# Kernel optimization log

Hardware: AMD Instinct MI355X
Metric: run time of the kernel (lower is better)

The kernel has to match this reference:

```python
import jax, jax.numpy as jnp
import numpy as np

NUM_HEADS = 16
H_SELF = 10  # hardcoded h in forward: first 10 heads self-attend, rest cross-attend
DIM = 1024
HEAD_DIM = DIM // NUM_HEADS
SCALE = HEAD_DIM ** -0.5


def _qkv(x, Wqkv):
    # x: [B, N, C] -> q, k, v each [B, H, N, hd]
    B, N, C = x.shape
    qkv = (x @ Wqkv).reshape(B, N, 3, NUM_HEADS, C // NUM_HEADS).transpose(2, 0, 3, 1, 4)
    return qkv[0], qkv[1], qkv[2]


def _attn(q, k, v):
    # q,k,v: [B, h, N, d]
    scores = jnp.einsum('bhqd,bhkd->bhqk', q, k) * SCALE
    probs = jax.nn.softmax(scores, axis=-1)  # attn_drop_ratio = 0.0
    return jnp.einsum('bhqk,bhkd->bhqd', probs, v)


def _proj(xa, xb, Wproj, bproj):
    # xa: [B, 10, N, d], xb: [B, 6, N, d] -> [B, N, C]
    B = xa.shape[0]
    N = xa.shape[2]
    x = jnp.concatenate([xa, xb], axis=1).transpose(0, 2, 1, 3).reshape(B, N, DIM)
    return x @ Wproj + bproj  # proj_drop_ratio = 0.0


def setup_inputs() -> dict:
    key = jax.random.key(0)
    k0, k1, k2, k3 = jax.random.split(key, 4)
    B, N, C = 16, 577, DIM
    x1 = jax.random.normal(k0, (B, N, C), dtype=jnp.float32)
    x2 = jax.random.normal(k1, (B, N, C), dtype=jnp.float32)
    # nn.Linear(dim, dim*3, bias=False): store as [C, 3C] so y = x @ W
    Wqkv = jax.random.normal(k2, (C, 3 * C), dtype=jnp.float32) * 0.02
    # nn.Linear(dim, dim) has bias by default
    Wproj = jax.random.normal(k3, (C, C), dtype=jnp.float32) * 0.02
    bproj = jnp.zeros((C,), dtype=jnp.float32)
    return {"x1": x1, "x2": x2, "Wqkv": Wqkv, "Wproj": Wproj, "bproj": bproj}


def reference(x1, x2, Wqkv, Wproj, bproj):
    q1, k1, v1 = _qkv(x1, Wqkv)
    q2, k2, v2 = _qkv(x2, Wqkv)
    h = H_SELF
    x11 = _attn(q1[:, :h], k1[:, :h], v1[:, :h])  # self-attn branch of x1
    x12 = _attn(q1[:, h:], k2[:, h:], v2[:, h:])  # cross: q from x1, kv from x2
    x22 = _attn(q2[:, :h], k2[:, :h], v2[:, :h])  # self-attn branch of x2
    x21 = _attn(q2[:, h:], k1[:, h:], v1[:, h:])  # cross: q from x2, kv from x1
    out1 = _proj(x11, x12, Wproj, bproj)
    out2 = _proj(x22, x21, Wproj, bproj)
    return (out1, out2)
```

## Files before the change

kernel.cpp:

```cpp
#include <hip/hip_runtime.h>
#include <hip/hip_bf16.h>
#include <stdint.h>
#include <math.h>

typedef __attribute__((ext_vector_type(8))) short bf16x8;
typedef __attribute__((ext_vector_type(4))) float f32x4;
typedef __attribute__((ext_vector_type(8))) unsigned short ushort8;
typedef __attribute__((ext_vector_type(4))) unsigned int uint4v;
typedef __attribute__((ext_vector_type(2))) unsigned int uint2v;

#define NTOK   9232
#define MROWS  18464
#define MPAD   18560
#define NPADV  640
#define QSCALE 0.18033688011112042f

__device__ __forceinline__ uint16_t f2b(float f) {
  uint32_t u = __builtin_bit_cast(uint32_t, f);
  u += 0x7fffu + ((u >> 16) & 1u);
  return (uint16_t)(u >> 16);
}

__device__ __forceinline__ uint32_t packbf(float lo, float hi) {
  return (uint32_t)f2b(lo) | ((uint32_t)f2b(hi) << 16);
}

__device__ __forceinline__ f32x4 mfma16(bf16x8 a, bf16x8 b, f32x4 c) {
  return __builtin_amdgcn_mfma_f32_16x16x32_bf16(a, b, c, 0, 0, 0);
}

__device__ __forceinline__ void gl_lds16(const void* g, void* l) {
  __builtin_amdgcn_global_load_lds(
      (const __attribute__((address_space(1))) uint32_t*)g,
      (__attribute__((address_space(3))) uint32_t*)l, 16, 0, 0);
}

__global__ void convert_x_kernel(const float* __restrict__ x1,
                                 const float* __restrict__ x2,
                                 uint16_t* __restrict__ Xb) {
  const size_t stride = (size_t)gridDim.x * blockDim.x;
  const size_t total8 = (size_t)MPAD * 1024 / 8;
  for (size_t i = (size_t)blockIdx.x * blockDim.x + threadIdx.x; i < total8; i += stride) {
    const size_t e = i * 8;
    const size_t row = e >> 10;
    ushort8 ov;
    if (row < (size_t)MROWS) {
      const float* src = (row < (size_t)NTOK) ? (x1 + e) : (x2 + (e - (size_t)NTOK * 1024));
      float4 a = *(const float4*)(src);
      float4 b = *(const float4*)(src + 4);
      ov[0] = f2b(a.x); ov[1] = f2b(a.y); ov[2] = f2b(a.z); ov[3] = f2b(a.w);
      ov[4] = f2b(b.x); ov[5] = f2b(b.y); ov[6] = f2b(b.z); ov[7] = f2b(b.w);
    } else {
      ov = (ushort8)0;
    }
    *(ushort8*)(Xb + e) = ov;
  }
}

__global__ void transw_kernel(const float* __restrict__ in, uint16_t* __restrict__ out,
                              int R, int Cc) {
  __shared__ float t[32][33];
  const int r0 = blockIdx.x * 32, c0 = blockIdx.y * 32;
  const int tr = threadIdx.x >> 5, tc = threadIdx.x & 31;
#pragma unroll
  for (int i = 0; i < 4; ++i)
    t[tr + i * 8][tc] = in[(size_t)(r0 + tr + i * 8) * Cc + c0 + tc];
  __syncthreads();
#pragma unroll
  for (int i = 0; i < 4; ++i) {
    const int orow = c0 + tr + i * 8;
    out[(size_t)orow * R + r0 + tc] = f2b(t[tc][tr + i * 8]);
  }
}

__global__ __launch_bounds__(256) void gemm_qkv_kernel(
    const uint16_t* __restrict__ A, const uint16_t* __restrict__ Bt,
    uint16_t* __restrict__ Qb, uint16_t* __restrict__ Kb, uint16_t* __restrict__ Vtb) {
  __shared__ uint16_t As[128 * 32];
  __shared__ uint16_t Bs[128 * 32];
  const int tid = threadIdx.x;
  const int w = tid >> 6, l = tid & 63;
  const int c = l & 15, g = l >> 4;
  const int wgid = blockIdx.x;
  const int work = (wgid & 7) * 435 + (wgid >> 3);
  int bm, bn;
  {
    const int stripe = work / 144;
    if (stripe >= 24) { bm = 144; bn = work - 24 * 144; }
    else {
      const int r2 = work % 144;
      const int st8 = r2 / 48, r3 = r2 % 48;
      bm = stripe * 6 + r3 % 6;
      bn = st8 * 8 + r3 / 6;
    }
  }
  const int wm = w >> 1, wn = w & 1;
  f32x4 acc[4][4] = {};

  const int srow = w * 32 + (l >> 2);
  const int scolB = (l & 3) * 16;
  const char* aG = (const char*)(A + (size_t)bm * 128 * 1024);
  const char* bG = (const char*)(Bt + (size_t)bn * 128 * 1024);
  char* aL0 = (char*)As + srow * 64 + scolB;
  char* aL1 = (char*)As + (srow + 16) * 64 + scolB;
  char* bL0 = (char*)Bs + srow * 64 + scolB;
  char* bL1 = (char*)Bs + (srow + 16) * 64 + scolB;
  const char* aG0 = aG + (size_t)srow * 2048 + scolB;
  const char* aG1 = aG + (size_t)(srow + 16) * 2048 + scolB;
  const char* bG0 = bG + (size_t)srow * 2048 + scolB;
  const char* bG1 = bG + (size_t)(srow + 16) * 2048 + scolB;

  for (int ks = 0; ks < 1024; ks += 32) {
    gl_lds16(aG0 + ks * 2, aL0);
    gl_lds16(aG1 + ks * 2, aL1);
    gl_lds16(bG0 + ks * 2, bL0);
    gl_lds16(bG1 + ks * 2, bL1);
    __syncthreads();
    bf16x8 af[4], bfv[4];
#pragma unroll
    for (int mi = 0; mi < 4; ++mi)
      af[mi] = *(const bf16x8*)((const char*)As + (wm * 64 + mi * 16 + c) * 64 + g * 16);
#pragma unroll
    for (int ni = 0; ni < 4; ++ni)
      bfv[ni] = *(const bf16x8*)((const char*)Bs + (wn * 64 + ni * 16 + c) * 64 + g * 16);
#pragma unroll
    for (int mi = 0; mi < 4; ++mi)
#pragma unroll
      for (int ni = 0; ni < 4; ++ni)
        acc[mi][ni] = mfma16(af[mi], bfv[ni], acc[mi][ni]);
    __syncthreads();
  }

  const int sArea = bn >> 3;
#pragma unroll
  for (int mi = 0; mi < 4; ++mi) {
#pragma unroll
    for (int r = 0; r < 4; ++r) {
      const int R = bm * 128 + wm * 64 + mi * 16 + g * 4 + r;
      if (R >= MROWS) continue;
      const int src = (R >= NTOK) ? 1 : 0;
      const int rr = R - src * NTOK;
      const int bb = rr / 577;
      const int nn = rr - bb * 577;
#pragma unroll
      for (int ni = 0; ni < 4; ++ni) {
        const int C = bn * 128 + wn * 64 + ni * 16 + c;
        const int c10 = C & 1023;
        const int hh = c10 >> 6, dd = c10 & 63;
        const size_t bh = ((size_t)src * 16 + bb) * 16 + hh;
        const float v = acc[mi][ni][r];
        if (sArea == 0)
          Qb[(bh * 577 + nn) * 64 + dd] = f2b(v * QSCALE);
        else if (sArea == 1)
          Kb[(bh * 577 + nn) * 64 + dd] = f2b(v);
        else
          Vtb[(bh * 64 + dd) * NPADV + nn] = f2b(v);
      }
    }
  }
}

#define KVB 64
#define ATT_NT 10
__global__ __launch_bounds__(256, 2) void attn_kernel(
    const uint16_t* __restrict__ Qb, const uint16_t* __restrict__ Kb,
    const uint16_t* __restrict__ Vtb, uint16_t* __restrict__ O) {
  __shared__ __align__(128) char smem[65536];
  const int tid = threadIdx.x;
  const int w = tid >> 6, l = tid & 63;
  const int c = l & 15, g = l >> 4;
  const int bid = blockIdx.x;
  const int qc = bid % 3;
  const int p = bid / 3;
  const int h = p & 15, b = (p >> 4) & 15, o = p >> 8;
  const int kvsrc = (h < 10) ? o : (1 - o);
  const uint16_t* qp = Qb + (((size_t)o * 16 + b) * 16 + h) * 577 * 64;
  const uint16_t* kp = Kb + (((size_t)kvsrc * 16 + b) * 16 + h) * 577 * 64;
  const uint16_t* vp = Vtb + (((size_t)kvsrc * 16 + b) * 16 + h) * 64 * NPADV;

  const int qbase = qc * 256 + w * 64;
  const bool active = (qbase <= 576);

  const int sub = l >> 3;
  const int colEl = (((l & 7) ^ sub) << 3);
  char* KsA = smem;
  char* VsA = smem + 16384;
  char* Pb  = smem + 32768 + w * 8192;
  const int rs = (c & 7) << 4;

  bf16x8 Qf[4][2];
  if (active) {
#pragma unroll
    for (int qt = 0; qt < 4; ++qt) {
      const int qrow = min(qbase + qt * 16 + c, 576);
      const uint16_t* qr = qp + (size_t)qrow * 64 + g * 8;
      Qf[qt][0] = *(const bf16x8*)(qr);
      Qf[qt][1] = *(const bf16x8*)(qr + 32);
    }
  }

  f32x4 acc[4][4] = {};
  float m_run[4] = {-3.0e38f, -3.0e38f, -3.0e38f, -3.0e38f};
  float l_run[4] = {0.f, 0.f, 0.f, 0.f};

  auto STAGE = [&](int buf, int kv0) {
#pragma unroll
    for (int i = 0; i < 2; ++i) {
      const int j = w * 2 + i;
      const int row = j * 8 + sub;
      const int gk = min(kv0 + row, 576);
      gl_lds16(kp + (size_t)gk * 64 + colEl, KsA + buf * 8192 + j * 1024 + l * 16);
      gl_lds16(vp + (size_t)row * NPADV + kv0 + colEl, VsA + buf * 8192 + j * 1024 + l * 16);
    }
  };

  STAGE(0, 0);
  __syncthreads();

  for (int t = 0; t < ATT_NT; ++t) {
    if (t < ATT_NT - 1) STAGE((t + 1) & 1, (t + 1) * KVB);
    if (active) {
      const char* Kt = KsA + (t & 1) * 8192;
      const char* Vt = VsA + (t & 1) * 8192;
      bf16x8 Kf[4][2];
#pragma unroll
      for (int kt = 0; kt < 4; ++kt) {
        const char* kr = Kt + (kt * 16 + c) * 128;
        Kf[kt][0] = *(const bf16x8*)(kr + ((g * 16) ^ rs));
        Kf[kt][1] = *(const bf16x8*)(kr + ((64 + g * 16) ^ rs));
      }
      float alpha_[4];
#pragma unroll
      for (int qt = 0; qt < 4; ++qt) {
        f32x4 s[4];
#pragma unroll
        for (int kt = 0; kt < 4; ++kt) {
          f32x4 z = {0.f, 0.f, 0.f, 0.f};
          z = mfma16(Kf[kt][0], Qf[qt][0], z);
          z = mfma16(Kf[kt][1], Qf[qt][1], z);
          s[kt] = z;
        }
        if (t == ATT_NT - 1) {
#pragma unroll
          for (int kt = 0; kt < 4; ++kt)
#pragma unroll
            for (int r = 0; r < 4; ++r) {
              if (kt == 0 && r == 0) { if (g > 0) s[kt][r] = -3.0e38f; }
              else s[kt][r] = -3.0e38f;
            }
        }
        float mt = s[0][0];
#pragma unroll
        for (int kt = 0; kt < 4; ++kt)
#pragma unroll
          for (int r = 0; r < 4; ++r) mt = fmaxf(mt, s[kt][r]);
        mt = fmaxf(mt, __shfl_xor(mt, 16));
        mt = fmaxf(mt, __shfl_xor(mt, 32));
        const float mnew = fmaxf(m_run[qt], mt);
        const float al = exp2f(m_run[qt] - mnew);
        m_run[qt] = mnew;
        alpha_[qt] = al;
        float lt = 0.f;
#pragma unroll
        for (int kt = 0; kt < 4; ++kt)
#pragma unroll
          for (int r = 0; r < 4; ++r) {
            const float pv = exp2f(s[kt][r] - mnew);
            s[kt][r] = pv;
            lt += pv;
          }
        lt += __shfl_xor(lt, 16);
        lt += __shfl_xor(lt, 32);
        l_run[qt] = l_run[qt] * al + lt;
        const int rowOff = (qt * 16 + c) * 128;
#pragma unroll
        for (int kt = 0; kt < 4; ++kt) {
          const uint2v pw = {packbf(s[kt][0], s[kt][1]), packbf(s[kt][2], s[kt][3])};
          *(uint2v*)(Pb + rowOff + ((kt * 32 + g * 8) ^ rs)) = pw;
        }
      }
#pragma unroll
      for (int dt = 0; dt < 4; ++dt)
#pragma unroll
        for (int qt = 0; qt < 4; ++qt)
#pragma unroll
          for (int r = 0; r < 4; ++r) acc[dt][qt][r] *= alpha_[qt];
      bf16x8 pf[4][2];
#pragma unroll
      for (int qt = 0; qt < 4; ++qt) {
        const char* pr = Pb + (qt * 16 + c) * 128;
        pf[qt][0] = *(const bf16x8*)(pr + ((g * 16) ^ rs));
        pf[qt][1] = *(const bf16x8*)(pr + ((64 + g * 16) ^ rs));
      }
#pragma unroll
      for (int dt = 0; dt < 4; ++dt) {
        const char* vr = Vt + (dt * 16 + c) * 128;
        const bf16x8 v0 = *(const bf16x8*)(vr + ((g * 16) ^ rs));
        const bf16x8 v1 = *(const bf16x8*)(vr + ((64 + g * 16) ^ rs));
#pragma unroll
        for (int qt = 0; qt < 4; ++qt) {
          acc[dt][qt] = mfma16(v0, pf[qt][0], acc[dt][qt]);
          acc[dt][qt] = mfma16(v1, pf[qt][1], acc[dt][qt]);
        }
      }
    }
    __syncthreads();
  }

  if (active) {
#pragma unroll
    for (int qt = 0; qt < 4; ++qt) {
      const float inv = 1.0f / l_run[qt];
      const int rowOff = (qt * 16 + c) * 128;
#pragma unroll
      for (int dt = 0; dt < 4; ++dt) {
        const uint2v pw = {packbf(acc[dt][qt][0] * inv, acc[dt][qt][1] * inv),
                           packbf(acc[dt][qt][2] * inv, acc[dt][qt][3] * inv)};
        *(uint2v*)(Pb + rowOff + ((dt * 32 + g * 8) ^ rs)) = pw;
      }
    }
    const size_t obase = ((size_t)o * NTOK + (size_t)b * 577) * 1024 + h * 64;
#pragma unroll
    for (int pass = 0; pass < 8; ++pass) {
      const int row = pass * 8 + (l >> 3);
      const int tok = qbase + row;
      const uint4v vv = *(const uint4v*)(Pb + row * 128 + (((l & 7) * 16) ^ ((row & 7) << 4)));
      if (tok <= 576)
        *(uint4v*)(O + obase + (size_t)tok * 1024 + (l & 7) * 8) = vv;
    }
  }
}

__global__ __launch_bounds__(256) void gemm_proj_kernel(
    const uint16_t* __restrict__ A, const uint16_t* __restrict__ Bt,
    const float* __restrict__ bias, float* __restrict__ out) {
  __shared__ uint16_t As[128 * 32];
  __shared__ uint16_t Bs[128 * 32];
  const int tid = threadIdx.x;
  const int w = tid >> 6, l = tid & 63;
  const int c = l & 15, g = l >> 4;
  const int wgid = blockIdx.x;
  const int work = (wgid & 7) * 145 + (wgid >> 3);
  int bm, bn;
  {
    const int stripe = work / 48;
    if (stripe >= 24) { bm = 144; bn = work - 24 * 48; }
    else { const int r3 = work % 48; bm = stripe * 6 + r3 % 6; bn = r3 / 6; }
  }
  const int wm = w >> 1, wn = w & 1;
  f32x4 acc[4][4] = {};

  const int srow = w * 32 + (l >> 2);
  const int scolB = (l & 3) * 16;
  const char* aG = (const char*)(A + (size_t)bm * 128 * 1024);
  const char* bG = (const char*)(Bt + (size_t)bn * 128 * 1024);
  char* aL0 = (char*)As + srow * 64 + scolB;
  char* aL1 = (char*)As + (srow + 16) * 64 + scolB;
  char* bL0 = (char*)Bs + srow * 64 + scolB;
  char* bL1 = (char*)Bs + (srow + 16) * 64 + scolB;
  const char* aG0 = aG + (size_t)srow * 2048 + scolB;
  const char* aG1 = aG + (size_t)(srow + 16) * 2048 + scolB;
  const char* bG0 = bG + (size_t)srow * 2048 + scolB;
  const char* bG1 = bG + (size_t)(srow + 16) * 2048 + scolB;

  for (int ks = 0; ks < 1024; ks += 32) {
    gl_lds16(aG0 + ks * 2, aL0);
    gl_lds16(aG1 + ks * 2, aL1);
    gl_lds16(bG0 + ks * 2, bL0);
    gl_lds16(bG1 + ks * 2, bL1);
    __syncthreads();
    bf16x8 af[4], bfv[4];
#pragma unroll
    for (int mi = 0; mi < 4; ++mi)
      af[mi] = *(const bf16x8*)((const char*)As + (wm * 64 + mi * 16 + c) * 64 + g * 16);
#pragma unroll
    for (int ni = 0; ni < 4; ++ni)
      bfv[ni] = *(const bf16x8*)((const char*)Bs + (wn * 64 + ni * 16 + c) * 64 + g * 16);
#pragma unroll
    for (int mi = 0; mi < 4; ++mi)
#pragma unroll
      for (int ni = 0; ni < 4; ++ni)
        acc[mi][ni] = mfma16(af[mi], bfv[ni], acc[mi][ni]);
    __syncthreads();
  }

#pragma unroll
  for (int mi = 0; mi < 4; ++mi) {
#pragma unroll
    for (int r = 0; r < 4; ++r) {
      const int R = bm * 128 + wm * 64 + mi * 16 + g * 4 + r;
      if (R >= MROWS) continue;
#pragma unroll
      for (int ni = 0; ni < 4; ++ni) {
        const int C = bn * 128 + wn * 64 + ni * 16 + c;
        out[(size_t)R * 1024 + C] = acc[mi][ni][r] + bias[C];
      }
    }
  }
}

extern "C" void kernel_launch(void* const* d_in, const int* in_sizes, int n_in,
                              void* d_out, int out_size, void* d_ws, size_t ws_size,
                              hipStream_t stream) {
  (void)in_sizes; (void)n_in; (void)out_size; (void)ws_size;
  const float* x1    = (const float*)d_in[0];
  const float* x2    = (const float*)d_in[1];
  const float* Wqkv  = (const float*)d_in[2];
  const float* Wproj = (const float*)d_in[3];
  const float* bproj = (const float*)d_in[4];
  float* out = (float*)d_out;

  char* ws = (char*)d_ws;
  size_t off = 0;
  auto alloc = [&](size_t bytes) -> char* {
    char* p = ws + off;
    off += (bytes + 255) & ~(size_t)255;
    return p;
  };
  uint16_t* Xb     = (uint16_t*)alloc((size_t)MPAD * 1024 * 2);
  uint16_t* Wqkvt  = (uint16_t*)alloc((size_t)3072 * 1024 * 2);
  uint16_t* Wprojt = (uint16_t*)alloc((size_t)1024 * 1024 * 2);
  uint16_t* Qb     = (uint16_t*)alloc((size_t)512 * 577 * 64 * 2);
  uint16_t* Kb     = (uint16_t*)alloc((size_t)512 * 577 * 64 * 2);
  const size_t vtBytes = (size_t)512 * 64 * NPADV * 2;
  uint16_t* Vtb    = (uint16_t*)alloc(vtBytes);

  hipMemsetAsync(Vtb, 0, vtBytes, stream);

  convert_x_kernel<<<2048, 256, 0, stream>>>(x1, x2, Xb);
  transw_kernel<<<dim3(32, 96), 256, 0, stream>>>(Wqkv, Wqkvt, 1024, 3072);
  transw_kernel<<<dim3(32, 32), 256, 0, stream>>>(Wproj, Wprojt, 1024, 1024);
  gemm_qkv_kernel<<<3480, 256, 0, stream>>>(Xb, Wqkvt, Qb, Kb, Vtb);
  attn_kernel<<<1536, 256, 0, stream>>>(Qb, Kb, Vtb, Xb );
  gemm_proj_kernel<<<1160, 256, 0, stream>>>(Xb, Wprojt, bproj, out);
}
```

Before: 424.8 us.

## Triple-buffer GEMM k-loop, rebalance attention rows, zero only V padding

Both GEMMs now use a three-stage LDS pipeline with XOR-swizzled tiles, explicit vmcnt waits, raw barriers and setprio around the MFMA block, replacing the single-buffer load/sync loop. This is meant to overlap global loads with compute and reduce LDS bank conflicts. The attention kernel goes from 3 query chunks of 256 rows to 2 chunks of 320 (80 rows per wave), which removes the idle waves of the last chunk at the cost of more registers and LDS per block. The full memset of the transposed V buffer is replaced by a small kernel that zeroes only the padding columns.

```diff
diff --git a/kernel.cpp b/kernel.cpp
--- a/kernel.cpp
+++ b/kernel.cpp
@@ -73,13 +73,83 @@
   }
 }
 
-__global__ __launch_bounds__(256) void gemm_qkv_kernel(
+__global__ void zero_vpad_kernel(uint16_t* __restrict__ Vtb) {
+  const int idx = blockIdx.x * 256 + threadIdx.x;
+  for (int i = idx; i < 32768 * 8; i += 256 * 256) {
+    const int p = i >> 3;
+    const int ch = i & 7;
+    *(ushort8*)(Vtb + (size_t)p * NPADV + 576 + ch * 8) = (ushort8)0;
+  }
+}
+
+#define GEMM_TRI_KLOOP                                                         \
+  const int srow4 = tt >> 2;                                        \
+  const int schunk = tt & 3;                         \
+  const int cr3 = c & 3;                                                       \
+  char* aL = (char*)As3;                                                       \
+  char* bL = (char*)Bs3;                                                       \
+  auto SA = [&](int buf, int t) {                                              \
+    _Pragma("unroll")                                                          \
+    for (int i = 0; i < 2; ++i) {                                              \
+      const int row = i * 64 + srow4;                                          \
+      gl_lds16(aG + (size_t)row * 2048 + t * 64 + ((schunk ^ (row & 3)) << 4), \
+               aL + buf * 8192 + row * 64 + (schunk << 4));                    \
+    }                                                                          \
+  };                                                                           \
+  auto SB = [&](int buf, int t) {                                              \
+    _Pragma("unroll")                                                          \
+    for (int i = 0; i < 2; ++i) {                                              \
+      const int row = i * 64 + srow4;                                          \
+      gl_lds16(bG + (size_t)row * 2048 + t * 64 + ((schunk ^ (row & 3)) << 4), \
+               bL + buf * 8192 + row * 64 + (schunk << 4));                    \
+    }                                                                          \
+  };                                                                           \
+  auto LDA = [&](int buf, int mi) -> bf16x8 {                                  \
+    const int r = wm * 64 + mi * 16 + c;                                       \
+    return *(const bf16x8*)(aL + buf * 8192 + r * 64 + ((g ^ cr3) << 4));      \
+  };                                                                           \
+  auto LDB = [&](int buf, int ni) -> bf16x8 {                                  \
+    const int r = wn * 64 + ni * 16 + c;                                       \
+    return *(const bf16x8*)(bL + buf * 8192 + r * 64 + ((g ^ cr3) << 4));      \
+  };                                                                           \
+  SA(0, 0); SB(0, 0); SA(1, 1); SB(1, 1);                                      \
+  int bufR = 0, bufS = 2;                                                      \
+  for (int t = 0; t < 32; ++t) {                                               \
+    if (t < 30) {                                                              \
+      SA(bufS, t + 2); SB(bufS, t + 2);                                        \
+      asm volatile("s_waitcnt vmcnt(8)" ::: "memory");                         \
+    } else if (t == 30) {                                                      \
+      asm volatile("s_waitcnt vmcnt(4)" ::: "memory");                         \
+    } else {                                                                   \
+      asm volatile("s_waitcnt vmcnt(0)" ::: "memory");                         \
+    }                                                                          \
+    __builtin_amdgcn_s_barrier();                                              \
+    __builtin_amdgcn_sched_barrier(0);                                         \
+    bf16x8 b0 = LDB(bufR, 0), b1 = LDB(bufR, 1);                               \
+    bf16x8 b2 = LDB(bufR, 2), b3 = LDB(bufR, 3);                               \
+    __builtin_amdgcn_s_setprio(1);                                             \
+    _Pragma("unroll")                                                          \
+    for (int mi = 0; mi < 4; ++mi) {                                           \
+      const bf16x8 a0 = LDA(bufR, mi);                                         \
+      acc[mi][0] = mfma16(a0, b0, acc[mi][0]);                                 \
+      acc[mi][1] = mfma16(a0, b1, acc[mi][1]);                                 \
+      acc[mi][2] = mfma16(a0, b2, acc[mi][2]);                                 \
+      acc[mi][3] = mfma16(a0, b3, acc[mi][3]);                                 \
+    }                                                                          \
+    __builtin_amdgcn_s_setprio(0);                                             \
+    __builtin_amdgcn_sched_barrier(0);                                         \
+    __builtin_amdgcn_s_barrier();                                              \
+    bufR = (bufR == 2) ? 0 : bufR + 1;                                         \
+    bufS = (bufS == 2) ? 0 : bufS + 1;                                         \
+  }
+
+__global__ __launch_bounds__(256, 3) void gemm_qkv_kernel(
     const uint16_t* __restrict__ A, const uint16_t* __restrict__ Bt,
     uint16_t* __restrict__ Qb, uint16_t* __restrict__ Kb, uint16_t* __restrict__ Vtb) {
-  __shared__ uint16_t As[128 * 32];
-  __shared__ uint16_t Bs[128 * 32];
-  const int tid = threadIdx.x;
-  const int w = tid >> 6, l = tid & 63;
+  __shared__ uint16_t As3[3][4096];
+  __shared__ uint16_t Bs3[3][4096];
+  const int tt = threadIdx.x;
+  const int w = tt >> 6, l = tt & 63;
   const int c = l & 15, g = l >> 4;
   const int wgid = blockIdx.x;
   const int work = (wgid & 7) * 435 + (wgid >> 3);
@@ -96,40 +166,10 @@
   }
   const int wm = w >> 1, wn = w & 1;
   f32x4 acc[4][4] = {};
-
-  const int srow = w * 32 + (l >> 2);
-  const int scolB = (l & 3) * 16;
   const char* aG = (const char*)(A + (size_t)bm * 128 * 1024);
   const char* bG = (const char*)(Bt + (size_t)bn * 128 * 1024);
-  char* aL0 = (char*)As + srow * 64 + scolB;
-  char* aL1 = (char*)As + (srow + 16) * 64 + scolB;
-  char* bL0 = (char*)Bs + srow * 64 + scolB;
-  char* bL1 = (char*)Bs + (srow + 16) * 64 + scolB;
-  const char* aG0 = aG + (size_t)srow * 2048 + scolB;
-  const char* aG1 = aG + (size_t)(srow + 16) * 2048 + scolB;
-  const char* bG0 = bG + (size_t)srow * 2048 + scolB;
-  const char* bG1 = bG + (size_t)(srow + 16) * 2048 + scolB;
-
-  for (int ks = 0; ks < 1024; ks += 32) {
-    gl_lds16(aG0 + ks * 2, aL0);
-    gl_lds16(aG1 + ks * 2, aL1);
-    gl_lds16(bG0 + ks * 2, bL0);
-    gl_lds16(bG1 + ks * 2, bL1);
-    __syncthreads();
-    bf16x8 af[4], bfv[4];
-#pragma unroll
-    for (int mi = 0; mi < 4; ++mi)
-      af[mi] = *(const bf16x8*)((const char*)As + (wm * 64 + mi * 16 + c) * 64 + g * 16);
-#pragma unroll
-    for (int ni = 0; ni < 4; ++ni)
-      bfv[ni] = *(const bf16x8*)((const char*)Bs + (wn * 64 + ni * 16 + c) * 64 + g * 16);
-#pragma unroll
-    for (int mi = 0; mi < 4; ++mi)
-#pragma unroll
-      for (int ni = 0; ni < 4; ++ni)
-        acc[mi][ni] = mfma16(af[mi], bfv[ni], acc[mi][ni]);
-    __syncthreads();
-  }
+
+  GEMM_TRI_KLOOP
 
   const int sArea = bn >> 3;
 #pragma unroll
@@ -165,43 +205,40 @@
 __global__ __launch_bounds__(256, 2) void attn_kernel(
     const uint16_t* __restrict__ Qb, const uint16_t* __restrict__ Kb,
     const uint16_t* __restrict__ Vtb, uint16_t* __restrict__ O) {
-  __shared__ __align__(128) char smem[65536];
+  __shared__ __align__(128) char smem[73728];
   const int tid = threadIdx.x;
   const int w = tid >> 6, l = tid & 63;
   const int c = l & 15, g = l >> 4;
   const int bid = blockIdx.x;
-  const int qc = bid % 3;
-  const int p = bid / 3;
+  const int qc = bid & 1;
+  const int p = bid >> 1;
   const int h = p & 15, b = (p >> 4) & 15, o = p >> 8;
   const int kvsrc = (h < 10) ? o : (1 - o);
   const uint16_t* qp = Qb + (((size_t)o * 16 + b) * 16 + h) * 577 * 64;
   const uint16_t* kp = Kb + (((size_t)kvsrc * 16 + b) * 16 + h) * 577 * 64;
   const uint16_t* vp = Vtb + (((size_t)kvsrc * 16 + b) * 16 + h) * 64 * NPADV;
 
-  const int qbase = qc * 256 + w * 64;
-  const bool active = (qbase <= 576);
+  const int qbase = qc * 320 + w * 80;
 
   const int sub = l >> 3;
   const int colEl = (((l & 7) ^ sub) << 3);
   char* KsA = smem;
   char* VsA = smem + 16384;
-  char* Pb  = smem + 32768 + w * 8192;
+  char* Pb  = smem + 32768 + w * 10240;
   const int rs = (c & 7) << 4;
 
-  bf16x8 Qf[4][2];
-  if (active) {
-#pragma unroll
-    for (int qt = 0; qt < 4; ++qt) {
-      const int qrow = min(qbase + qt * 16 + c, 576);
-      const uint16_t* qr = qp + (size_t)qrow * 64 + g * 8;
-      Qf[qt][0] = *(const bf16x8*)(qr);
-      Qf[qt][1] = *(const bf16x8*)(qr + 32);
-    }
-  }
-
-  f32x4 acc[4][4] = {};
-  float m_run[4] = {-3.0e38f, -3.0e38f, -3.0e38f, -3.0e38f};
-  float l_run[4] = {0.f, 0.f, 0.f, 0.f};
+  bf16x8 Qf[5][2];
+#pragma unroll
+  for (int qt = 0; qt < 5; ++qt) {
+    const int qrow = min(qbase + qt * 16 + c, 576);
+    const uint16_t* qr = qp + (size_t)qrow * 64 + g * 8;
+    Qf[qt][0] = *(const bf16x8*)(qr);
+    Qf[qt][1] = *(const bf16x8*)(qr + 32);
+  }
+
+  f32x4 acc[4][5] = {};
+  float m_run[5] = {-3.0e38f, -3.0e38f, -3.0e38f, -3.0e38f, -3.0e38f};
+  float l_run[5] = {0.f, 0.f, 0.f, 0.f, 0.f};
 
   auto STAGE = [&](int buf, int kv0) {
 #pragma unroll
@@ -219,7 +256,7 @@
 
   for (int t = 0; t < ATT_NT; ++t) {
     if (t < ATT_NT - 1) STAGE((t + 1) & 1, (t + 1) * KVB);
-    if (active) {
+    {
       const char* Kt = KsA + (t & 1) * 8192;
       const char* Vt = VsA + (t & 1) * 8192;
       bf16x8 Kf[4][2];
@@ -229,9 +266,9 @@
         Kf[kt][0] = *(const bf16x8*)(kr + ((g * 16) ^ rs));
         Kf[kt][1] = *(const bf16x8*)(kr + ((64 + g * 16) ^ rs));
       }
-      float alpha_[4];
-#pragma unroll
-      for (int qt = 0; qt < 4; ++qt) {
+      float alpha_[5];
+#pragma unroll
+      for (int qt = 0; qt < 5; ++qt) {
         f32x4 s[4];
 #pragma unroll
         for (int kt = 0; kt < 4; ++kt) {
@@ -282,12 +319,12 @@
 #pragma unroll
       for (int dt = 0; dt < 4; ++dt)
 #pragma unroll
-        for (int qt = 0; qt < 4; ++qt)
+        for (int qt = 0; qt < 5; ++qt)
 #pragma unroll
           for (int r = 0; r < 4; ++r) acc[dt][qt][r] *= alpha_[qt];
-      bf16x8 pf[4][2];
-#pragma unroll
-      for (int qt = 0; qt < 4; ++qt) {
+      bf16x8 pf[5][2];
+#pragma unroll
+      for (int qt = 0; qt < 5; ++qt) {
         const char* pr = Pb + (qt * 16 + c) * 128;
         pf[qt][0] = *(const bf16x8*)(pr + ((g * 16) ^ rs));
         pf[qt][1] = *(const bf16x8*)(pr + ((64 + g * 16) ^ rs));
@@ -298,7 +335,7 @@
         const bf16x8 v0 = *(const bf16x8*)(vr + ((g * 16) ^ rs));
         const bf16x8 v1 = *(const bf16x8*)(vr + ((64 + g * 16) ^ rs));
 #pragma unroll
-        for (int qt = 0; qt < 4; ++qt) {
+        for (int qt = 0; qt < 5; ++qt) {
           acc[dt][qt] = mfma16(v0, pf[qt][0], acc[dt][qt]);
           acc[dt][qt] = mfma16(v1, pf[qt][1], acc[dt][qt]);
         }
@@ -307,9 +344,9 @@
     __syncthreads();
   }
 
-  if (active) {
-#pragma unroll
-    for (int qt = 0; qt < 4; ++qt) {
+  {
+#pragma unroll
+    for (int qt = 0; qt < 5; ++qt) {
       const float inv = 1.0f / l_run[qt];
       const int rowOff = (qt * 16 + c) * 128;
 #pragma unroll
@@ -321,7 +358,7 @@
     }
     const size_t obase = ((size_t)o * NTOK + (size_t)b * 577) * 1024 + h * 64;
 #pragma unroll
-    for (int pass = 0; pass < 8; ++pass) {
+    for (int pass = 0; pass < 10; ++pass) {
       const int row = pass * 8 + (l >> 3);
       const int tok = qbase + row;
       const uint4v vv = *(const uint4v*)(Pb + row * 128 + (((l & 7) * 16) ^ ((row & 7) << 4)));
@@ -331,13 +368,13 @@
   }
 }
 
-__global__ __launch_bounds__(256) void gemm_proj_kernel(
+__global__ __launch_bounds__(256, 3) void gemm_proj_kernel(
     const uint16_t* __restrict__ A, const uint16_t* __restrict__ Bt,
     const float* __restrict__ bias, float* __restrict__ out) {
-  __shared__ uint16_t As[128 * 32];
-  __shared__ uint16_t Bs[128 * 32];
-  const int tid = threadIdx.x;
-  const int w = tid >> 6, l = tid & 63;
+  __shared__ uint16_t As3[3][4096];
+  __shared__ uint16_t Bs3[3][4096];
+  const int tt = threadIdx.x;
+  const int w = tt >> 6, l = tt & 63;
   const int c = l & 15, g = l >> 4;
   const int wgid = blockIdx.x;
   const int work = (wgid & 7) * 145 + (wgid >> 3);
@@ -349,40 +386,10 @@
   }
   const int wm = w >> 1, wn = w & 1;
   f32x4 acc[4][4] = {};
-
-  const int srow = w * 32 + (l >> 2);
-  const int scolB = (l & 3) * 16;
   const char* aG = (const char*)(A + (size_t)bm * 128 * 1024);
   const char* bG = (const char*)(Bt + (size_t)bn * 128 * 1024);
-  char* aL0 = (char*)As + srow * 64 + scolB;
-  char* aL1 = (char*)As + (srow + 16) * 64 + scolB;
-  char* bL0 = (char*)Bs + srow * 64 + scolB;
-  char* bL1 = (char*)Bs + (srow + 16) * 64 + scolB;
-  const char* aG0 = aG + (size_t)srow * 2048 + scolB;
-  const char* aG1 = aG + (size_t)(srow + 16) * 2048 + scolB;
-  const char* bG0 = bG + (size_t)srow * 2048 + scolB;
-  const char* bG1 = bG + (size_t)(srow + 16) * 2048 + scolB;
-
-  for (int ks = 0; ks < 1024; ks += 32) {
-    gl_lds16(aG0 + ks * 2, aL0);
-    gl_lds16(aG1 + ks * 2, aL1);
-    gl_lds16(bG0 + ks * 2, bL0);
-    gl_lds16(bG1 + ks * 2, bL1);
-    __syncthreads();
-    bf16x8 af[4], bfv[4];
-#pragma unroll
-    for (int mi = 0; mi < 4; ++mi)
-      af[mi] = *(const bf16x8*)((const char*)As + (wm * 64 + mi * 16 + c) * 64 + g * 16);
-#pragma unroll
-    for (int ni = 0; ni < 4; ++ni)
-      bfv[ni] = *(const bf16x8*)((const char*)Bs + (wn * 64 + ni * 16 + c) * 64 + g * 16);
-#pragma unroll
-    for (int mi = 0; mi < 4; ++mi)
-#pragma unroll
-      for (int ni = 0; ni < 4; ++ni)
-        acc[mi][ni] = mfma16(af[mi], bfv[ni], acc[mi][ni]);
-    __syncthreads();
-  }
+
+  GEMM_TRI_KLOOP
 
 #pragma unroll
   for (int mi = 0; mi < 4; ++mi) {
@@ -422,15 +429,13 @@
   uint16_t* Wprojt = (uint16_t*)alloc((size_t)1024 * 1024 * 2);
   uint16_t* Qb     = (uint16_t*)alloc((size_t)512 * 577 * 64 * 2);
   uint16_t* Kb     = (uint16_t*)alloc((size_t)512 * 577 * 64 * 2);
-  const size_t vtBytes = (size_t)512 * 64 * NPADV * 2;
-  uint16_t* Vtb    = (uint16_t*)alloc(vtBytes);
-
-  hipMemsetAsync(Vtb, 0, vtBytes, stream);
-
+  uint16_t* Vtb    = (uint16_t*)alloc((size_t)512 * 64 * NPADV * 2);
+
+  zero_vpad_kernel<<<256, 256, 0, stream>>>(Vtb);
   convert_x_kernel<<<2048, 256, 0, stream>>>(x1, x2, Xb);
   transw_kernel<<<dim3(32, 96), 256, 0, stream>>>(Wqkv, Wqkvt, 1024, 3072);
   transw_kernel<<<dim3(32, 32), 256, 0, stream>>>(Wproj, Wprojt, 1024, 1024);
   gemm_qkv_kernel<<<3480, 256, 0, stream>>>(Xb, Wqkvt, Qb, Kb, Vtb);
-  attn_kernel<<<1536, 256, 0, stream>>>(Qb, Kb, Vtb, Xb );
+  attn_kernel<<<1024, 256, 0, stream>>>(Qb, Kb, Vtb, Xb );
   gemm_proj_kernel<<<1160, 256, 0, stream>>>(Xb, Wprojt, bproj, out);
 }
```

Result: faster. 397.4 us (-6.4%).
